# Optimization experiments

Hardware: AMD Instinct MI355X
Metric: run time of the kernel (lower is better)

Reference implementation:

```python
import jax, jax.numpy as jnp
import numpy as np

N = 20000
E = 320000
IN_FEAT = 256
HID = 256
OUT_FEAT = 128


def setup_inputs() -> dict:
    key = jax.random.key(0)
    ks = jax.random.split(key, 10)
    inp = {
        "x": jax.random.normal(ks[0], (N, IN_FEAT), dtype=jnp.float32),
        "edge_src": jax.random.randint(ks[1], (E,), 0, N, dtype=jnp.int32),
        "edge_dst": jax.random.randint(ks[2], (E,), 0, N, dtype=jnp.int32),
        "edge_w": jax.random.uniform(ks[3], (E,), dtype=jnp.float32),
        # params (Linear weights stored as [out, in], torch convention)
        "W_emb": jax.random.normal(ks[4], (HID, IN_FEAT), dtype=jnp.float32) / np.sqrt(IN_FEAT),
        "W_gc1": jax.random.normal(ks[5], (HID, 2 * HID), dtype=jnp.float32) / np.sqrt(2 * HID),
        "b_gc1": jnp.zeros((HID,), dtype=jnp.float32),
        "W_gc2": jax.random.normal(ks[6], (HID, 2 * HID), dtype=jnp.float32) / np.sqrt(2 * HID),
        "b_gc2": jnp.zeros((HID,), dtype=jnp.float32),
        "W_fc": jax.random.normal(ks[7], (OUT_FEAT, HID), dtype=jnp.float32) / np.sqrt(HID),
    }
    return inp


def reference(x, edge_src, edge_dst, edge_w, W_emb, W_gc1, b_gc1, W_gc2, b_gc2, W_fc):
    n = x.shape[0]

    def adj_mul(h):
        msgs = h[edge_src] * edge_w[:, None]           # [E, hid]
        return jax.ops.segment_sum(msgs, edge_dst, num_segments=n)

    def gconv(h, W, b):
        cat = jnp.concatenate([h, adj_mul(h)], axis=1)  # [N, 2*hid]
        return cat @ W.T + b

    h = x @ W_emb.T                                    # embedding (no bias)
    h = h + jax.nn.relu(gconv(h, W_gc1, b_gc1))        # residual (dropout = eval identity)
    h = h + jax.nn.relu(gconv(h, W_gc2, b_gc2))
    out = h @ W_fc.T                                   # fc_last (no bias)
    out = out / jnp.sqrt(jnp.sum(out * out, axis=1, keepdims=True))
    return out
```

## Files before the change

### kernel.cpp

```cpp
#include <hip/hip_runtime.h>
#include <math.h>

#define N_NODES 20000
#define E_EDGES 320000
#define HID 256
#define OUT_FEAT 128
#define MPAD 20224
#define CAP 64

#define BK 64
#define LSTR 72
#define TSTR 264

typedef __attribute__((ext_vector_type(8))) __bf16 bf16x8;
typedef __attribute__((ext_vector_type(4))) float floatx4;

__device__ __forceinline__ void write_int8_shadow(
    const __bf16 (*tile)[TSTR], int row0, int tid,
    unsigned char* __restrict__ h8, float* __restrict__ scl) {
    const int row = tid >> 3;
    const int seg = tid & 7;
    float vals[32];
    float mx = 0.f;
#pragma unroll
    for (int j = 0; j < 32; j++) {
        float v = (float)tile[row][seg * 32 + j];
        vals[j] = v;
        mx = fmaxf(mx, fabsf(v));
    }
#pragma unroll
    for (int m = 1; m <= 4; m <<= 1) mx = fmaxf(mx, __shfl_xor(mx, m));
    const float enc = mx > 0.f ? 127.f / mx : 0.f;
    unsigned int pk[8];
#pragma unroll
    for (int g = 0; g < 8; g++) {
        unsigned int wd = 0;
#pragma unroll
        for (int j = 0; j < 4; j++) {
            int q = (int)rintf(vals[g * 4 + j] * enc);
            q = q > 127 ? 127 : (q < -127 ? -127 : q);
            wd |= ((unsigned int)(q & 0xff)) << (8 * j);
        }
        pk[g] = wd;
    }
    unsigned char* dstp = h8 + (size_t)(row0 + row) * HID + seg * 32;
    *(int4*)dstp        = make_int4(pk[0], pk[1], pk[2], pk[3]);
    *(int4*)(dstp + 16) = make_int4(pk[4], pk[5], pk[6], pk[7]);
    if (seg == 0) scl[row0 + row] = mx * (1.f / 127.f);
}


#define EMB_BLK 316
#define SCAT_BLK 625
#define CONV_BLK 72

__global__ __launch_bounds__(512) void front_kernel(
    const float* __restrict__ x,
    const float* __restrict__ wembf,
    __bf16* __restrict__ hb0,
    unsigned char* __restrict__ h8,
    float* __restrict__ scl,
    const int* __restrict__ src, const int* __restrict__ dst,
    const float* __restrict__ w, int* __restrict__ counts,
    int2* __restrict__ edges,
    const float* __restrict__ w1f, const float* __restrict__ w2f,
    const float* __restrict__ wfcf,
    __bf16* __restrict__ w1b, __bf16* __restrict__ w2b,
    __bf16* __restrict__ wfcb)
{
    __shared__ __bf16 smem[64 * LSTR + 256 * LSTR];
    const int bid = blockIdx.x;
    const int tid = threadIdx.x;

    if (bid < EMB_BLK) {
        __bf16* As = smem;
        __bf16* Bs = smem + 64 * LSTR;
        const int row0 = bid * 64;
        const int wv = tid >> 6, l = tid & 63, lr = l & 15, lq = l >> 4;
        const int wm = wv & 1, wn4 = wv >> 1;

        floatx4 acc[2][4];
#pragma unroll
        for (int i = 0; i < 2; i++)
#pragma unroll
            for (int j = 0; j < 4; j++) acc[i][j] = (floatx4){0.f, 0.f, 0.f, 0.f};

        const int srow = tid >> 3;
        const int skq = (tid & 7) * 8;

        for (int kc = 0; kc < 256; kc += BK) {
            {
                int grow = row0 + srow;
                float4 v0 = make_float4(0.f, 0.f, 0.f, 0.f), v1 = v0;
                if (grow < N_NODES) {
                    const float* xp = x + (size_t)grow * HID + kc + skq;
                    v0 = *(const float4*)xp;
                    v1 = *(const float4*)(xp + 4);
                }
                bf16x8 o;
                o[0] = (__bf16)v0.x; o[1] = (__bf16)v0.y; o[2] = (__bf16)v0.z; o[3] = (__bf16)v0.w;
                o[4] = (__bf16)v1.x; o[5] = (__bf16)v1.y; o[6] = (__bf16)v1.z; o[7] = (__bf16)v1.w;
                *(bf16x8*)&As[srow * LSTR + skq] = o;
            }
#pragma unroll
            for (int r = 0; r < 4; r++) {
                int row = r * 64 + srow;
                const float* wp = wembf + (size_t)row * 256 + kc + skq;
                float4 v0 = *(const float4*)wp;
                float4 v1 = *(const float4*)(wp + 4);
                bf16x8 o;
                o[0] = (__bf16)v0.x; o[1] = (__bf16)v0.y; o[2] = (__bf16)v0.z; o[3] = (__bf16)v0.w;
                o[4] = (__bf16)v1.x; o[5] = (__bf16)v1.y; o[6] = (__bf16)v1.z; o[7] = (__bf16)v1.w;
                *(bf16x8*)&Bs[row * LSTR + skq] = o;
            }
            __syncthreads();
#pragma unroll
            for (int s = 0; s < 2; s++) {
                bf16x8 af[2], bfr[4];
#pragma unroll
                for (int mt = 0; mt < 2; mt++)
                    af[mt] = *(const bf16x8*)&As[(wm * 32 + mt * 16 + lr) * LSTR + s * 32 + lq * 8];
#pragma unroll
                for (int nt = 0; nt < 4; nt++)
                    bfr[nt] = *(const bf16x8*)&Bs[(wn4 * 64 + nt * 16 + lr) * LSTR + s * 32 + lq * 8];
#pragma unroll
                for (int mt = 0; mt < 2; mt++)
#pragma unroll
                    for (int nt = 0; nt < 4; nt++)
                        acc[mt][nt] = __builtin_amdgcn_mfma_f32_16x16x32_bf16(af[mt], bfr[nt], acc[mt][nt], 0, 0, 0);
            }
            __syncthreads();
        }
        __bf16 (*tile)[TSTR] = (__bf16(*)[TSTR])smem;
#pragma unroll
        for (int nt = 0; nt < 4; nt++) {
            const int col = wn4 * 64 + nt * 16 + lr;
#pragma unroll
            for (int mt = 0; mt < 2; mt++) {
                const int lrow = wm * 32 + mt * 16 + lq * 4;
#pragma unroll
                for (int r = 0; r < 4; r++) {
                    float v = acc[mt][nt][r];
                    hb0[(size_t)(row0 + lrow + r) * HID + col] = (__bf16)v;
                    tile[lrow + r][col] = (__bf16)v;
                }
            }
        }
        __syncthreads();
        write_int8_shadow(tile, row0, tid, h8, scl);
    } else if (bid < EMB_BLK + SCAT_BLK) {
        int e = (bid - EMB_BLK) * 512 + tid;
        int d = dst[e];
        int p = atomicAdd(&counts[d], 1);
        edges[(size_t)d * CAP + p] = make_int2(src[e], __float_as_int(w[e]));
    } else {
        const size_t gi = ((size_t)(bid - EMB_BLK - SCAT_BLK) * 512 + tid) * 8;
        const size_t s1 = 131072, s2 = 262144;
        const float* srcp; __bf16* dstp; size_t off;
        if (gi < s1)      { srcp = w1f; dstp = w1b; off = gi; }
        else if (gi < s2) { srcp = w2f; dstp = w2b; off = gi - s1; }
        else              { srcp = wfcf; dstp = wfcb; off = gi - s2; }
        float4 v0 = *(const float4*)(srcp + off);
        float4 v1 = *(const float4*)(srcp + off + 4);
        bf16x8 o;
        o[0] = (__bf16)v0.x; o[1] = (__bf16)v0.y; o[2] = (__bf16)v0.z; o[3] = (__bf16)v0.w;
        o[4] = (__bf16)v1.x; o[5] = (__bf16)v1.y; o[6] = (__bf16)v1.z; o[7] = (__bf16)v1.w;
        *(bf16x8*)(dstp + off) = o;
    }
}


__global__ __launch_bounds__(256) void aggregate_kernel(
    const unsigned char* __restrict__ h8, const float* __restrict__ scl,
    const int* __restrict__ counts,
    const int2* __restrict__ edges, __bf16* __restrict__ agg) {
    const int w = threadIdx.x >> 6, lane = threadIdx.x & 63;
    const int half = lane >> 5, lh = lane & 31;
    const int d = blockIdx.x * 8 + w * 2 + half;
    const size_t base = (size_t)d * CAP;
    const int cnt = counts[d];
    const int iters = (cnt + 15) >> 4;
    float acc[8];
#pragma unroll
    for (int q = 0; q < 8; q++) acc[q] = 0.f;

    for (int it = 0; it < iters; ++it) {
        const int jb = it * 16;
        const int2* ep = edges + base + jb;
        int4 eh[8];
#pragma unroll
        for (int u = 0; u < 8; u++) eh[u] = *(const int4*)(ep + u * 2);
        int sidx[16]; float ew[16];
#pragma unroll
        for (int u = 0; u < 8; u++) {
            const bool m0 = (jb + u * 2)     < cnt;
            const bool m1 = (jb + u * 2 + 1) < cnt;
            sidx[u * 2]     = m0 ? eh[u].x : 0;
            ew[u * 2]       = m0 ? __int_as_float(eh[u].y) : 0.f;
            sidx[u * 2 + 1] = m1 ? eh[u].z : 0;
            ew[u * 2 + 1]   = m1 ? __int_as_float(eh[u].w) : 0.f;
        }
        float ws[16];
#pragma unroll
        for (int u = 0; u < 16; u++) ws[u] = ew[u] * scl[sidx[u]];
        uint2 hv[16];
#pragma unroll
        for (int u = 0; u < 16; u++)
            hv[u] = *(const uint2*)(h8 + (size_t)sidx[u] * HID + lh * 8);
#pragma unroll
        for (int u = 0; u < 16; u++) {
            const unsigned int a = hv[u].x, b = hv[u].y;
            const float wu = ws[u];
            acc[0] = fmaf(wu, (float)(int)(signed char)(a),       acc[0]);
            acc[1] = fmaf(wu, (float)(int)(signed char)(a >> 8),  acc[1]);
            acc[2] = fmaf(wu, (float)(int)(signed char)(a >> 16), acc[2]);
            acc[3] = fmaf(wu, (float)(int)(signed char)(a >> 24), acc[3]);
            acc[4] = fmaf(wu, (float)(int)(signed char)(b),       acc[4]);
            acc[5] = fmaf(wu, (float)(int)(signed char)(b >> 8),  acc[5]);
            acc[6] = fmaf(wu, (float)(int)(signed char)(b >> 16), acc[6]);
            acc[7] = fmaf(wu, (float)(int)(signed char)(b >> 24), acc[7]);
        }
    }
    bf16x8 o;
#pragma unroll
    for (int q = 0; q < 8; q++) o[q] = (__bf16)acc[q];
    *(bf16x8*)(agg + (size_t)d * HID + lh * 8) = o;
}


__global__ __launch_bounds__(512) void gconv1_kernel(
    const __bf16* __restrict__ hp,
    const __bf16* __restrict__ ag,
    const __bf16* __restrict__ W,
    const float* __restrict__ bias,
    __bf16* __restrict__ hn,
    unsigned char* __restrict__ h8,
    float* __restrict__ scl)
{
    __shared__ __bf16 smem[64 * LSTR + 256 * LSTR];
    __bf16* As = smem;
    __bf16* Bs = smem + 64 * LSTR;
    const int tid = threadIdx.x;
    const int row0 = blockIdx.x * 64;
    const int wv = tid >> 6, l = tid & 63, lr = l & 15, lq = l >> 4;
    const int wm = wv & 1, wn4 = wv >> 1;

    floatx4 acc[2][4];
#pragma unroll
    for (int i = 0; i < 2; i++)
#pragma unroll
        for (int j = 0; j < 4; j++) acc[i][j] = (floatx4){0.f, 0.f, 0.f, 0.f};

    const int srow = tid >> 3;
    const int skq = (tid & 7) * 8;

    for (int kc = 0; kc < 512; kc += BK) {
        const __bf16* Asrc = (kc >= 256) ? ag : hp;
        const int ks = kc & 255;
        *(bf16x8*)&As[srow * LSTR + skq] =
            *(const bf16x8*)(Asrc + (size_t)(row0 + srow) * HID + ks + skq);
#pragma unroll
        for (int r = 0; r < 4; r++) {
            int row = r * 64 + srow;
            *(bf16x8*)&Bs[row * LSTR + skq] =
                *(const bf16x8*)(W + (size_t)row * 512 + kc + skq);
        }
        __syncthreads();
#pragma unroll
        for (int s = 0; s < 2; s++) {
            bf16x8 af[2], bfr[4];
#pragma unroll
            for (int mt = 0; mt < 2; mt++)
                af[mt] = *(const bf16x8*)&As[(wm * 32 + mt * 16 + lr) * LSTR + s * 32 + lq * 8];
#pragma unroll
            for (int nt = 0; nt < 4; nt++)
                bfr[nt] = *(const bf16x8*)&Bs[(wn4 * 64 + nt * 16 + lr) * LSTR + s * 32 + lq * 8];
#pragma unroll
            for (int mt = 0; mt < 2; mt++)
#pragma unroll
                for (int nt = 0; nt < 4; nt++)
                    acc[mt][nt] = __builtin_amdgcn_mfma_f32_16x16x32_bf16(af[mt], bfr[nt], acc[mt][nt], 0, 0, 0);
        }
        __syncthreads();
    }

    __bf16 (*tile)[TSTR] = (__bf16(*)[TSTR])smem;
#pragma unroll
    for (int nt = 0; nt < 4; nt++) {
        const int col = wn4 * 64 + nt * 16 + lr;
        const float b = bias[col];
#pragma unroll
        for (int mt = 0; mt < 2; mt++) {
            const int lrow = wm * 32 + mt * 16 + lq * 4;
#pragma unroll
            for (int r = 0; r < 4; r++) {
                float res = (float)hp[(size_t)(row0 + lrow + r) * HID + col];
                float v = res + fmaxf(acc[mt][nt][r] + b, 0.f);
                hn[(size_t)(row0 + lrow + r) * HID + col] = (__bf16)v;
                tile[lrow + r][col] = (__bf16)v;
            }
        }
    }
    __syncthreads();
    write_int8_shadow(tile, row0, tid, h8, scl);
}


__global__ __launch_bounds__(512) void gconv_fc_kernel(
    const __bf16* __restrict__ hp,
    const __bf16* __restrict__ ag,
    const __bf16* __restrict__ W,
    const float* __restrict__ bias,
    const __bf16* __restrict__ Wfc,
    float* __restrict__ outp)
{
    __shared__ __bf16 smem[64 * LSTR + 256 * LSTR];
    __bf16* As = smem;
    __bf16* Bs = smem + 64 * LSTR;
    const int tid = threadIdx.x;
    const int row0 = blockIdx.x * 64;
    const int wv = tid >> 6, l = tid & 63, lr = l & 15, lq = l >> 4;
    const int wm = wv & 1, wn4 = wv >> 1;

    floatx4 acc[2][4];
#pragma unroll
    for (int i = 0; i < 2; i++)
#pragma unroll
        for (int j = 0; j < 4; j++) acc[i][j] = (floatx4){0.f, 0.f, 0.f, 0.f};

    const int srow = tid >> 3;
    const int skq = (tid & 7) * 8;

    for (int kc = 0; kc < 512; kc += BK) {
        const __bf16* Asrc = (kc >= 256) ? ag : hp;
        const int ks = kc & 255;
        *(bf16x8*)&As[srow * LSTR + skq] =
            *(const bf16x8*)(Asrc + (size_t)(row0 + srow) * HID + ks + skq);
#pragma unroll
        for (int r = 0; r < 4; r++) {
            int row = r * 64 + srow;
            *(bf16x8*)&Bs[row * LSTR + skq] =
                *(const bf16x8*)(W + (size_t)row * 512 + kc + skq);
        }
        __syncthreads();
#pragma unroll
        for (int s = 0; s < 2; s++) {
            bf16x8 af[2], bfr[4];
#pragma unroll
            for (int mt = 0; mt < 2; mt++)
                af[mt] = *(const bf16x8*)&As[(wm * 32 + mt * 16 + lr) * LSTR + s * 32 + lq * 8];
#pragma unroll
            for (int nt = 0; nt < 4; nt++)
                bfr[nt] = *(const bf16x8*)&Bs[(wn4 * 64 + nt * 16 + lr) * LSTR + s * 32 + lq * 8];
#pragma unroll
            for (int mt = 0; mt < 2; mt++)
#pragma unroll
                for (int nt = 0; nt < 4; nt++)
                    acc[mt][nt] = __builtin_amdgcn_mfma_f32_16x16x32_bf16(af[mt], bfr[nt], acc[mt][nt], 0, 0, 0);
        }
        __syncthreads();
    }

    __bf16 (*tile)[TSTR] = (__bf16(*)[TSTR])smem;
#pragma unroll
    for (int nt = 0; nt < 4; nt++) {
        const int col = wn4 * 64 + nt * 16 + lr;
        const float b = bias[col];
#pragma unroll
        for (int mt = 0; mt < 2; mt++) {
            const int lrow = wm * 32 + mt * 16 + lq * 4;
#pragma unroll
            for (int r = 0; r < 4; r++) {
                float res = (float)hp[(size_t)(row0 + lrow + r) * HID + col];
                float v = res + fmaxf(acc[mt][nt][r] + b, 0.f);
                tile[lrow + r][col] = (__bf16)v;
            }
        }
    }
    __syncthreads();

    if (wv < 4) {
        floatx4 facc[8];
#pragma unroll
        for (int j = 0; j < 8; j++) facc[j] = (floatx4){0.f, 0.f, 0.f, 0.f};
#pragma unroll
        for (int kt = 0; kt < 256; kt += 32) {
            bf16x8 a = *(const bf16x8*)&tile[wv * 16 + lr][kt + lq * 8];
            bf16x8 bf8[8];
#pragma unroll
            for (int nt = 0; nt < 8; nt++)
                bf8[nt] = *(const bf16x8*)(Wfc + (size_t)(nt * 16 + lr) * 256 + kt + lq * 8);
#pragma unroll
            for (int nt = 0; nt < 8; nt++)
                facc[nt] = __builtin_amdgcn_mfma_f32_16x16x32_bf16(a, bf8[nt], facc[nt], 0, 0, 0);
        }
        float s[4];
#pragma unroll
        for (int r = 0; r < 4; r++) {
            float t = 0.f;
#pragma unroll
            for (int nt = 0; nt < 8; nt++) t = fmaf(facc[nt][r], facc[nt][r], t);
            s[r] = t;
        }
#pragma unroll
        for (int mask = 1; mask <= 8; mask <<= 1) {
#pragma unroll
            for (int r = 0; r < 4; r++) s[r] += __shfl_xor(s[r], mask);
        }
        float inv[4];
#pragma unroll
        for (int r = 0; r < 4; r++) inv[r] = rsqrtf(s[r]);
#pragma unroll
        for (int r = 0; r < 4; r++) {
            int row = row0 + wv * 16 + lq * 4 + r;
            if (row >= N_NODES) continue;
#pragma unroll
            for (int nt = 0; nt < 8; nt++)
                outp[(size_t)row * OUT_FEAT + nt * 16 + lr] = facc[nt][r] * inv[r];
        }
    }
}


extern "C" void kernel_launch(void* const* d_in, const int* in_sizes, int n_in,
                              void* d_out, int out_size, void* d_ws, size_t ws_size,
                              hipStream_t stream) {
    const float* x        = (const float*)d_in[0];
    const int*   edge_src = (const int*)d_in[1];
    const int*   edge_dst = (const int*)d_in[2];
    const float* edge_w   = (const float*)d_in[3];
    const float* W_emb    = (const float*)d_in[4];
    const float* W_gc1    = (const float*)d_in[5];
    const float* b_gc1    = (const float*)d_in[6];
    const float* W_gc2    = (const float*)d_in[7];
    const float* b_gc2    = (const float*)d_in[8];
    const float* W_fc     = (const float*)d_in[9];
    float* out = (float*)d_out;

    char* p = (char*)d_ws;
    const size_t HROW = (size_t)MPAD * HID;
    __bf16* hb0   = (__bf16*)p;             p += HROW * 2;
    __bf16* hb1   = (__bf16*)p;             p += HROW * 2;
    __bf16* aggb  = (__bf16*)p;             p += HROW * 2;
    unsigned char* h8 = (unsigned char*)p;  p += HROW;
    float*  scl   = (float*)p;              p += (size_t)MPAD * 4;
    __bf16* w1b   = (__bf16*)p;             p += 131072 * 2;
    __bf16* w2b   = (__bf16*)p;             p += 131072 * 2;
    __bf16* wfcb  = (__bf16*)p;             p += 32768 * 2;
    int2*   edges = (int2*)p;               p += (size_t)N_NODES * CAP * 8;
    int*    counts = (int*)p;               p += (size_t)MPAD * 4;

    hipMemsetAsync(counts, 0, (size_t)MPAD * 4, stream);

    front_kernel<<<EMB_BLK + SCAT_BLK + CONV_BLK, 512, 0, stream>>>(
        x, W_emb, hb0, h8, scl, edge_src, edge_dst, edge_w, counts, edges,
        W_gc1, W_gc2, W_fc, w1b, w2b, wfcb);

    aggregate_kernel<<<N_NODES / 8, 256, 0, stream>>>(h8, scl, counts, edges, aggb);

    gconv1_kernel<<<MPAD / 64, 512, 0, stream>>>(hb0, aggb, w1b, b_gc1, hb1, h8, scl);

    aggregate_kernel<<<N_NODES / 8, 256, 0, stream>>>(h8, scl, counts, edges, aggb);

    gconv_fc_kernel<<<MPAD / 64, 512, 0, stream>>>(hb1, aggb, w2b, b_gc2, wfcb, out);
}
```

Before: 202.8 us.

## Quantize aggregated features and right weight half to int8, use int8 MFMA

The aggregate kernel now writes per-row int8-quantized outputs with a float scale instead of bf16. The right (neighbour) half of each gconv weight is quantized per output row to int8 in the front kernel. The gconv GEMM splits into a bf16 MFMA pass over the self half and an int8 MFMA pass over the aggregated half, combined with the row and column scales. This halves the bytes for the aggregate buffer and the right-half weights and uses the faster int8 matrix instructions, at the cost of extra quantization error. The two gconv kernels are merged into one template.

```diff
diff --git a/kernel.cpp b/kernel.cpp
--- a/kernel.cpp
+++ b/kernel.cpp
@@ -10,10 +10,12 @@
 
 #define BK 64
 #define LSTR 72
+#define ISTR 80
 #define TSTR 264
 
 typedef __attribute__((ext_vector_type(8))) __bf16 bf16x8;
 typedef __attribute__((ext_vector_type(4))) float floatx4;
+typedef __attribute__((ext_vector_type(4))) int intx4;
 
 __device__ __forceinline__ void write_int8_shadow(
     const __bf16 (*tile)[TSTR], int row0, int tid,
@@ -52,29 +54,26 @@
 
 #define EMB_BLK 316
 #define SCAT_BLK 625
-#define CONV_BLK 72
+#define CONVL_BLK 40
+#define CONVR_BLK 64
 
 __global__ __launch_bounds__(512) void front_kernel(
-    const float* __restrict__ x,
-    const float* __restrict__ wembf,
-    __bf16* __restrict__ hb0,
-    unsigned char* __restrict__ h8,
-    float* __restrict__ scl,
+    const float* __restrict__ x, const float* __restrict__ wembf,
+    __bf16* __restrict__ hb0, unsigned char* __restrict__ h8, float* __restrict__ scl,
     const int* __restrict__ src, const int* __restrict__ dst,
-    const float* __restrict__ w, int* __restrict__ counts,
-    int2* __restrict__ edges,
-    const float* __restrict__ w1f, const float* __restrict__ w2f,
-    const float* __restrict__ wfcf,
-    __bf16* __restrict__ w1b, __bf16* __restrict__ w2b,
-    __bf16* __restrict__ wfcb)
+    const float* __restrict__ w, int* __restrict__ counts, int2* __restrict__ edges,
+    const float* __restrict__ w1f, const float* __restrict__ w2f, const float* __restrict__ wfcf,
+    __bf16* __restrict__ w1l, __bf16* __restrict__ w2l, __bf16* __restrict__ wfcb,
+    unsigned char* __restrict__ w1r8, unsigned char* __restrict__ w2r8,
+    float* __restrict__ w1rs, float* __restrict__ w2rs)
 {
-    __shared__ __bf16 smem[64 * LSTR + 256 * LSTR];
+    __shared__ char smem[64 * 144 + 256 * 144];
     const int bid = blockIdx.x;
     const int tid = threadIdx.x;
 
     if (bid < EMB_BLK) {
-        __bf16* As = smem;
-        __bf16* Bs = smem + 64 * LSTR;
+        __bf16* As = (__bf16*)smem;
+        __bf16* Bs = (__bf16*)(smem + 64 * 144);
         const int row0 = bid * 64;
         const int wv = tid >> 6, l = tid & 63, lr = l & 15, lq = l >> 4;
         const int wm = wv & 1, wn4 = wv >> 1;
@@ -153,19 +152,47 @@
         int d = dst[e];
         int p = atomicAdd(&counts[d], 1);
         edges[(size_t)d * CAP + p] = make_int2(src[e], __float_as_int(w[e]));
-    } else {
+    } else if (bid < EMB_BLK + SCAT_BLK + CONVL_BLK) {
         const size_t gi = ((size_t)(bid - EMB_BLK - SCAT_BLK) * 512 + tid) * 8;
-        const size_t s1 = 131072, s2 = 262144;
-        const float* srcp; __bf16* dstp; size_t off;
-        if (gi < s1)      { srcp = w1f; dstp = w1b; off = gi; }
-        else if (gi < s2) { srcp = w2f; dstp = w2b; off = gi - s1; }
-        else              { srcp = wfcf; dstp = wfcb; off = gi - s2; }
-        float4 v0 = *(const float4*)(srcp + off);
-        float4 v1 = *(const float4*)(srcp + off + 4);
+        const float* sp; __bf16* dp;
+        if (gi < 65536) {
+            size_t row = gi >> 8, k = gi & 255;
+            sp = w1f + row * 512 + k; dp = w1l + gi;
+        } else if (gi < 131072) {
+            size_t off = gi - 65536, row = off >> 8, k = off & 255;
+            sp = w2f + row * 512 + k; dp = w2l + off;
+        } else {
+            size_t off = gi - 131072;
+            sp = wfcf + off; dp = wfcb + off;
+        }
+        float4 v0 = *(const float4*)sp;
+        float4 v1 = *(const float4*)(sp + 4);
         bf16x8 o;
         o[0] = (__bf16)v0.x; o[1] = (__bf16)v0.y; o[2] = (__bf16)v0.z; o[3] = (__bf16)v0.w;
         o[4] = (__bf16)v1.x; o[5] = (__bf16)v1.y; o[6] = (__bf16)v1.z; o[7] = (__bf16)v1.w;
-        *(bf16x8*)(dstp + off) = o;
+        *(bf16x8*)dp = o;
+    } else {
+        const int gw = (bid - EMB_BLK - SCAT_BLK - CONVL_BLK) * 8 + (tid >> 6);
+        const int lane = tid & 63;
+        const float* Wsrc = (gw < 256) ? w1f : w2f;
+        unsigned char* d8 = (gw < 256) ? w1r8 : w2r8;
+        float* ds = (gw < 256) ? w1rs : w2rs;
+        const int r = gw & 255;
+        float4 v = *(const float4*)(Wsrc + (size_t)r * 512 + 256 + lane * 4);
+        float mx = fmaxf(fmaxf(fabsf(v.x), fabsf(v.y)), fmaxf(fabsf(v.z), fabsf(v.w)));
+#pragma unroll
+        for (int m = 1; m <= 32; m <<= 1) mx = fmaxf(mx, __shfl_xor(mx, m));
+        const float enc = mx > 0.f ? 127.f / mx : 0.f;
+        unsigned int wd = 0;
+        float vv[4] = {v.x, v.y, v.z, v.w};
+#pragma unroll
+        for (int j = 0; j < 4; j++) {
+            int q = (int)rintf(vv[j] * enc);
+            q = q > 127 ? 127 : (q < -127 ? -127 : q);
+            wd |= ((unsigned int)(q & 0xff)) << (8 * j);
+        }
+        *(unsigned int*)(d8 + (size_t)r * 256 + lane * 4) = wd;
+        if (lane == 0) ds[r] = mx * (1.f / 127.f);
     }
 }
 
@@ -173,7 +200,8 @@
 __global__ __launch_bounds__(256) void aggregate_kernel(
     const unsigned char* __restrict__ h8, const float* __restrict__ scl,
     const int* __restrict__ counts,
-    const int2* __restrict__ edges, __bf16* __restrict__ agg) {
+    const int2* __restrict__ edges,
+    unsigned char* __restrict__ agg8, float* __restrict__ ascl) {
     const int w = threadIdx.x >> 6, lane = threadIdx.x & 63;
     const int half = lane >> 5, lh = lane & 31;
     const int d = blockIdx.x * 8 + w * 2 + half;
@@ -221,49 +249,68 @@
             acc[7] = fmaf(wu, (float)(int)(signed char)(b >> 24), acc[7]);
         }
     }
-    bf16x8 o;
-#pragma unroll
-    for (int q = 0; q < 8; q++) o[q] = (__bf16)acc[q];
-    *(bf16x8*)(agg + (size_t)d * HID + lh * 8) = o;
+    float mx = 0.f;
+#pragma unroll
+    for (int q = 0; q < 8; q++) mx = fmaxf(mx, fabsf(acc[q]));
+#pragma unroll
+    for (int m = 1; m <= 16; m <<= 1) mx = fmaxf(mx, __shfl_xor(mx, m));
+    const float enc = mx > 0.f ? 127.f / mx : 0.f;
+    unsigned int w0 = 0, w1v = 0;
+#pragma unroll
+    for (int j = 0; j < 4; j++) {
+        int q0 = (int)rintf(acc[j] * enc);
+        q0 = q0 > 127 ? 127 : (q0 < -127 ? -127 : q0);
+        w0 |= ((unsigned int)(q0 & 0xff)) << (8 * j);
+        int q1 = (int)rintf(acc[4 + j] * enc);
+        q1 = q1 > 127 ? 127 : (q1 < -127 ? -127 : q1);
+        w1v |= ((unsigned int)(q1 & 0xff)) << (8 * j);
+    }
+    *(uint2*)(agg8 + (size_t)d * HID + lh * 8) = make_uint2(w0, w1v);
+    if (lh == 0) ascl[d] = mx * (1.f / 127.f);
 }
 
 
-__global__ __launch_bounds__(512) void gconv1_kernel(
+template <bool LAST>
+__global__ __launch_bounds__(512) void gconv_kernel(
     const __bf16* __restrict__ hp,
-    const __bf16* __restrict__ ag,
-    const __bf16* __restrict__ W,
+    const unsigned char* __restrict__ ag8, const float* __restrict__ ascl,
+    const __bf16* __restrict__ Wl,
+    const unsigned char* __restrict__ Wr8, const float* __restrict__ Wrs,
     const float* __restrict__ bias,
-    __bf16* __restrict__ hn,
-    unsigned char* __restrict__ h8,
-    float* __restrict__ scl)
+    __bf16* __restrict__ hn, unsigned char* __restrict__ h8, float* __restrict__ scl,
+    const __bf16* __restrict__ Wfc, float* __restrict__ outp)
 {
-    __shared__ __bf16 smem[64 * LSTR + 256 * LSTR];
-    __bf16* As = smem;
-    __bf16* Bs = smem + 64 * LSTR;
+    __shared__ char smem[64 * 144 + 256 * 144];
+    __bf16* As = (__bf16*)smem;
+    __bf16* Bs = (__bf16*)(smem + 64 * 144);
+    char* As8 = smem;
+    char* Bs8 = smem + 64 * ISTR;
     const int tid = threadIdx.x;
     const int row0 = blockIdx.x * 64;
     const int wv = tid >> 6, l = tid & 63, lr = l & 15, lq = l >> 4;
     const int wm = wv & 1, wn4 = wv >> 1;
 
     floatx4 acc[2][4];
+    intx4 acc8[2][4];
 #pragma unroll
     for (int i = 0; i < 2; i++)
 #pragma unroll
-        for (int j = 0; j < 4; j++) acc[i][j] = (floatx4){0.f, 0.f, 0.f, 0.f};
+        for (int j = 0; j < 4; j++) {
+            acc[i][j] = (floatx4){0.f, 0.f, 0.f, 0.f};
+            acc8[i][j] = (intx4){0, 0, 0, 0};
+        }
 
     const int srow = tid >> 3;
     const int skq = (tid & 7) * 8;
 
-    for (int kc = 0; kc < 512; kc += BK) {
-        const __bf16* Asrc = (kc >= 256) ? ag : hp;
-        const int ks = kc & 255;
+    for (int kc = 0; kc < 256; kc += BK) {
         *(bf16x8*)&As[srow * LSTR + skq] =
-            *(const bf16x8*)(Asrc + (size_t)(row0 + srow) * HID + ks + skq);
+            *(const bf16x8*)(hp + (size_t)(row0 + srow) * HID + kc + skq);
 #pragma unroll
         for (int r = 0; r < 4; r++) {
             int row = r * 64 + srow;
             *(bf16x8*)&Bs[row * LSTR + skq] =
-                *(const bf16x8*)(W + (size_t)row * 512 + kc + skq);
+                *(const bf16x8*)(Wl + (size_t)row * 256 + kc + skq);
         }
         __syncthreads();
 #pragma unroll
@@ -281,6 +328,35 @@
                 for (int nt = 0; nt < 4; nt++)
                     acc[mt][nt] = __builtin_amdgcn_mfma_f32_16x16x32_bf16(af[mt], bfr[nt], acc[mt][nt], 0, 0, 0);
         }
+        __syncthreads();
+    }
+
+    for (int kc = 0; kc < 256; kc += BK) {
+        {
+            int row = tid >> 3, sg = (tid & 7) * 8;
+            *(uint2*)&As8[row * ISTR + sg] =
+                *(const uint2*)(ag8 + (size_t)(row0 + row) * HID + kc + sg);
+        }
+#pragma unroll
+        for (int rr = 0; rr < 2; rr++) {
+            int idx = rr * 512 + tid;
+            int row = idx >> 2, sg = (idx & 3) * 16;
+            *(int4*)&Bs8[row * ISTR + sg] =
+                *(const int4*)(Wr8 + (size_t)row * 256 + kc + sg);
+        }
+        __syncthreads();
+        intx4 a8[2], b8[4];
+#pragma unroll
+        for (int mt = 0; mt < 2; mt++)
+            a8[mt] = *(const intx4*)&As8[(wm * 32 + mt * 16 + lr) * ISTR + lq * 16];
+#pragma unroll
+        for (int nt = 0; nt < 4; nt++)
+            b8[nt] = *(const intx4*)&Bs8[(wn4 * 64 + nt * 16 + lr) * ISTR + lq * 16];
+#pragma unroll
+        for (int mt = 0; mt < 2; mt++)
+#pragma unroll
+            for (int nt = 0; nt < 4; nt++)
+                acc8[mt][nt] = __builtin_amdgcn_mfma_i32_16x16x64_i8(a8[mt], b8[nt], acc8[mt][nt], 0, 0, 0);
         __syncthreads();
     }
 
@@ -289,97 +365,26 @@
     for (int nt = 0; nt < 4; nt++) {
         const int col = wn4 * 64 + nt * 16 + lr;
         const float b = bias[col];
+        const float wrc = Wrs[col];
 #pragma unroll
         for (int mt = 0; mt < 2; mt++) {
             const int lrow = wm * 32 + mt * 16 + lq * 4;
 #pragma unroll
             for (int r = 0; r < 4; r++) {
-                float res = (float)hp[(size_t)(row0 + lrow + r) * HID + col];
-                float v = res + fmaxf(acc[mt][nt][r] + b, 0.f);
-                hn[(size_t)(row0 + lrow + r) * HID + col] = (__bf16)v;
+                const int row = row0 + lrow + r;
+                float gem = acc[mt][nt][r] + (float)acc8[mt][nt][r] * (ascl[row] * wrc);
+                float res = (float)hp[(size_t)row * HID + col];
+                float v = res + fmaxf(gem + b, 0.f);
+                if (!LAST) hn[(size_t)row * HID + col] = (__bf16)v;
                 tile[lrow + r][col] = (__bf16)v;
             }
         }
     }
     __syncthreads();
-    write_int8_shadow(tile, row0, tid, h8, scl);
-}
-
-
-__global__ __launch_bounds__(512) void gconv_fc_kernel(
-    const __bf16* __restrict__ hp,
-    const __bf16* __restrict__ ag,
-    const __bf16* __restrict__ W,
-    const float* __restrict__ bias,
-    const __bf16* __restrict__ Wfc,
-    float* __restrict__ outp)
-{
-    __shared__ __bf16 smem[64 * LSTR + 256 * LSTR];
-    __bf16* As = smem;
-    __bf16* Bs = smem + 64 * LSTR;
-    const int tid = threadIdx.x;
-    const int row0 = blockIdx.x * 64;
-    const int wv = tid >> 6, l = tid & 63, lr = l & 15, lq = l >> 4;
-    const int wm = wv & 1, wn4 = wv >> 1;
-
-    floatx4 acc[2][4];
-#pragma unroll
-    for (int i = 0; i < 2; i++)
-#pragma unroll
-        for (int j = 0; j < 4; j++) acc[i][j] = (floatx4){0.f, 0.f, 0.f, 0.f};
-
-    const int srow = tid >> 3;
-    const int skq = (tid & 7) * 8;
-
-    for (int kc = 0; kc < 512; kc += BK) {
-        const __bf16* Asrc = (kc >= 256) ? ag : hp;
-        const int ks = kc & 255;
-        *(bf16x8*)&As[srow * LSTR + skq] =
-            *(const bf16x8*)(Asrc + (size_t)(row0 + srow) * HID + ks + skq);
-#pragma unroll
-        for (int r = 0; r < 4; r++) {
-            int row = r * 64 + srow;
-            *(bf16x8*)&Bs[row * LSTR + skq] =
-                *(const bf16x8*)(W + (size_t)row * 512 + kc + skq);
-        }
-        __syncthreads();
-#pragma unroll
-        for (int s = 0; s < 2; s++) {
-            bf16x8 af[2], bfr[4];
-#pragma unroll
-            for (int mt = 0; mt < 2; mt++)
-                af[mt] = *(const bf16x8*)&As[(wm * 32 + mt * 16 + lr) * LSTR + s * 32 + lq * 8];
-#pragma unroll
-            for (int nt = 0; nt < 4; nt++)
-                bfr[nt] = *(const bf16x8*)&Bs[(wn4 * 64 + nt * 16 + lr) * LSTR + s * 32 + lq * 8];
-#pragma unroll
-            for (int mt = 0; mt < 2; mt++)
-#pragma unroll
-                for (int nt = 0; nt < 4; nt++)
-                    acc[mt][nt] = __builtin_amdgcn_mfma_f32_16x16x32_bf16(af[mt], bfr[nt], acc[mt][nt], 0, 0, 0);
-        }
-        __syncthreads();
-    }
-
-    __bf16 (*tile)[TSTR] = (__bf16(*)[TSTR])smem;
-#pragma unroll
-    for (int nt = 0; nt < 4; nt++) {
-        const int col = wn4 * 64 + nt * 16 + lr;
-        const float b = bias[col];
-#pragma unroll
-        for (int mt = 0; mt < 2; mt++) {
-            const int lrow = wm * 32 + mt * 16 + lq * 4;
-#pragma unroll
-            for (int r = 0; r < 4; r++) {
-                float res = (float)hp[(size_t)(row0 + lrow + r) * HID + col];
-                float v = res + fmaxf(acc[mt][nt][r] + b, 0.f);
-                tile[lrow + r][col] = (__bf16)v;
-            }
-        }
-    }
-    __syncthreads();
-
-    if (wv < 4) {
+
+    if (!LAST) {
+        write_int8_shadow(tile, row0, tid, h8, scl);
+    } else if (wv < 4) {
         floatx4 facc[8];
 #pragma unroll
         for (int j = 0; j < 8; j++) facc[j] = (floatx4){0.f, 0.f, 0.f, 0.f};
@@ -441,26 +446,33 @@
     const size_t HROW = (size_t)MPAD * HID;
     __bf16* hb0   = (__bf16*)p;             p += HROW * 2;
     __bf16* hb1   = (__bf16*)p;             p += HROW * 2;
-    __bf16* aggb  = (__bf16*)p;             p += HROW * 2;
     unsigned char* h8 = (unsigned char*)p;  p += HROW;
     float*  scl   = (float*)p;              p += (size_t)MPAD * 4;
-    __bf16* w1b   = (__bf16*)p;             p += 131072 * 2;
-    __bf16* w2b   = (__bf16*)p;             p += 131072 * 2;
+    unsigned char* agg8 = (unsigned char*)p; p += HROW;
+    float*  ascl  = (float*)p;              p += (size_t)MPAD * 4;
+    __bf16* w1l   = (__bf16*)p;             p += 65536 * 2;
+    __bf16* w2l   = (__bf16*)p;             p += 65536 * 2;
     __bf16* wfcb  = (__bf16*)p;             p += 32768 * 2;
+    unsigned char* w1r8 = (unsigned char*)p; p += 65536;
+    unsigned char* w2r8 = (unsigned char*)p; p += 65536;
+    float*  w1rs  = (float*)p;              p += 256 * 4;
+    float*  w2rs  = (float*)p;              p += 256 * 4;
     int2*   edges = (int2*)p;               p += (size_t)N_NODES * CAP * 8;
     int*    counts = (int*)p;               p += (size_t)MPAD * 4;
 
     hipMemsetAsync(counts, 0, (size_t)MPAD * 4, stream);
 
-    front_kernel<<<EMB_BLK + SCAT_BLK + CONV_BLK, 512, 0, stream>>>(
+    front_kernel<<<EMB_BLK + SCAT_BLK + CONVL_BLK + CONVR_BLK, 512, 0, stream>>>(
         x, W_emb, hb0, h8, scl, edge_src, edge_dst, edge_w, counts, edges,
-        W_gc1, W_gc2, W_fc, w1b, w2b, wfcb);
-
-    aggregate_kernel<<<N_NODES / 8, 256, 0, stream>>>(h8, scl, counts, edges, aggb);
-
-    gconv1_kernel<<<MPAD / 64, 512, 0, stream>>>(hb0, aggb, w1b, b_gc1, hb1, h8, scl);
-
-    aggregate_kernel<<<N_NODES / 8, 256, 0, stream>>>(h8, scl, counts, edges, aggb);
-
-    gconv_fc_kernel<<<MPAD / 64, 512, 0, stream>>>(hb1, aggb, w2b, b_gc2, wfcb, out);
+        W_gc1, W_gc2, W_fc, w1l, w2l, wfcb, w1r8, w2r8, w1rs, w2rs);
+
+    aggregate_kernel<<<N_NODES / 8, 256, 0, stream>>>(h8, scl, counts, edges, agg8, ascl);
+
+    gconv_kernel<false><<<MPAD / 64, 512, 0, stream>>>(
+        hb0, agg8, ascl, w1l, w1r8, w1rs, b_gc1, hb1, h8, scl, nullptr, nullptr);
+
+    aggregate_kernel<<<N_NODES / 8, 256, 0, stream>>>(h8, scl, counts, edges, agg8, ascl);
+
+    gconv_kernel<true><<<MPAD / 64, 512, 0, stream>>>(
+        hb1, agg8, ascl, w2l, w2r8, w2rs, b_gc2, nullptr, nullptr, nullptr, wfcb, out);
 }
```

New measurement: 202.5 us. Within noise of the previous version (-0.1%).

## Overlap edge aggregation with identity-half GEMM in a combined kernel

Applied to the files above, without the earlier changes.

Each graph-conv layer's GEMM is split into two halves. The half that multiplies h by the left 256 columns of W has no dependence on the aggregation, so it now runs as extra blocks inside the aggregation kernel and writes fp32 partial sums to a new workspace buffer. The follow-up kernel computes only the aggregated half and adds the partials before bias, ReLU and residual, which lets the GEMM overlap with the memory-latency-bound gather. The cost is an extra fp32 round-trip of an N×256 buffer, and the aggregation waves now process 8 edges per iteration instead of 16.

```diff
diff --git a/kernel.cpp b/kernel.cpp
--- a/kernel.cpp
+++ b/kernel.cpp
@@ -55,18 +55,12 @@
 #define CONV_BLK 72
 
 __global__ __launch_bounds__(512) void front_kernel(
-    const float* __restrict__ x,
-    const float* __restrict__ wembf,
-    __bf16* __restrict__ hb0,
-    unsigned char* __restrict__ h8,
-    float* __restrict__ scl,
+    const float* __restrict__ x, const float* __restrict__ wembf,
+    __bf16* __restrict__ hb0, unsigned char* __restrict__ h8, float* __restrict__ scl,
     const int* __restrict__ src, const int* __restrict__ dst,
-    const float* __restrict__ w, int* __restrict__ counts,
-    int2* __restrict__ edges,
-    const float* __restrict__ w1f, const float* __restrict__ w2f,
-    const float* __restrict__ wfcf,
-    __bf16* __restrict__ w1b, __bf16* __restrict__ w2b,
-    __bf16* __restrict__ wfcb)
+    const float* __restrict__ w, int* __restrict__ counts, int2* __restrict__ edges,
+    const float* __restrict__ w1f, const float* __restrict__ w2f, const float* __restrict__ wfcf,
+    __bf16* __restrict__ w1b, __bf16* __restrict__ w2b, __bf16* __restrict__ wfcb)
 {
     __shared__ __bf16 smem[64 * LSTR + 256 * LSTR];
     const int bid = blockIdx.x;
@@ -156,86 +150,152 @@
     } else {
         const size_t gi = ((size_t)(bid - EMB_BLK - SCAT_BLK) * 512 + tid) * 8;
         const size_t s1 = 131072, s2 = 262144;
-        const float* srcp; __bf16* dstp; size_t off;
-        if (gi < s1)      { srcp = w1f; dstp = w1b; off = gi; }
-        else if (gi < s2) { srcp = w2f; dstp = w2b; off = gi - s1; }
-        else              { srcp = wfcf; dstp = wfcb; off = gi - s2; }
-        float4 v0 = *(const float4*)(srcp + off);
-        float4 v1 = *(const float4*)(srcp + off + 4);
+        const float* sp; __bf16* dp; size_t off;
+        if (gi < s1)      { sp = w1f; dp = w1b; off = gi; }
+        else if (gi < s2) { sp = w2f; dp = w2b; off = gi - s1; }
+        else              { sp = wfcf; dp = wfcb; off = gi - s2; }
+        float4 v0 = *(const float4*)(sp + off);
+        float4 v1 = *(const float4*)(sp + off + 4);
         bf16x8 o;
         o[0] = (__bf16)v0.x; o[1] = (__bf16)v0.y; o[2] = (__bf16)v0.z; o[3] = (__bf16)v0.w;
         o[4] = (__bf16)v1.x; o[5] = (__bf16)v1.y; o[6] = (__bf16)v1.z; o[7] = (__bf16)v1.w;
-        *(bf16x8*)(dstp + off) = o;
+        *(bf16x8*)(dp + off) = o;
     }
 }
 
 
-__global__ __launch_bounds__(256) void aggregate_kernel(
+#define AGG_BLK 1250
+
+__global__ __launch_bounds__(512) void agg_gemmL_kernel(
     const unsigned char* __restrict__ h8, const float* __restrict__ scl,
-    const int* __restrict__ counts,
-    const int2* __restrict__ edges, __bf16* __restrict__ agg) {
-    const int w = threadIdx.x >> 6, lane = threadIdx.x & 63;
-    const int half = lane >> 5, lh = lane & 31;
-    const int d = blockIdx.x * 8 + w * 2 + half;
-    const size_t base = (size_t)d * CAP;
-    const int cnt = counts[d];
-    const int iters = (cnt + 15) >> 4;
-    float acc[8];
-#pragma unroll
-    for (int q = 0; q < 8; q++) acc[q] = 0.f;
-
-    for (int it = 0; it < iters; ++it) {
-        const int jb = it * 16;
-        const int2* ep = edges + base + jb;
-        int4 eh[8];
-#pragma unroll
-        for (int u = 0; u < 8; u++) eh[u] = *(const int4*)(ep + u * 2);
-        int sidx[16]; float ew[16];
-#pragma unroll
-        for (int u = 0; u < 8; u++) {
-            const bool m0 = (jb + u * 2)     < cnt;
-            const bool m1 = (jb + u * 2 + 1) < cnt;
-            sidx[u * 2]     = m0 ? eh[u].x : 0;
-            ew[u * 2]       = m0 ? __int_as_float(eh[u].y) : 0.f;
-            sidx[u * 2 + 1] = m1 ? eh[u].z : 0;
-            ew[u * 2 + 1]   = m1 ? __int_as_float(eh[u].w) : 0.f;
-        }
-        float ws[16];
-#pragma unroll
-        for (int u = 0; u < 16; u++) ws[u] = ew[u] * scl[sidx[u]];
-        uint2 hv[16];
-#pragma unroll
-        for (int u = 0; u < 16; u++)
-            hv[u] = *(const uint2*)(h8 + (size_t)sidx[u] * HID + lh * 8);
-#pragma unroll
-        for (int u = 0; u < 16; u++) {
-            const unsigned int a = hv[u].x, b = hv[u].y;
-            const float wu = ws[u];
-            acc[0] = fmaf(wu, (float)(int)(signed char)(a),       acc[0]);
-            acc[1] = fmaf(wu, (float)(int)(signed char)(a >> 8),  acc[1]);
-            acc[2] = fmaf(wu, (float)(int)(signed char)(a >> 16), acc[2]);
-            acc[3] = fmaf(wu, (float)(int)(signed char)(a >> 24), acc[3]);
-            acc[4] = fmaf(wu, (float)(int)(signed char)(b),       acc[4]);
-            acc[5] = fmaf(wu, (float)(int)(signed char)(b >> 8),  acc[5]);
-            acc[6] = fmaf(wu, (float)(int)(signed char)(b >> 16), acc[6]);
-            acc[7] = fmaf(wu, (float)(int)(signed char)(b >> 24), acc[7]);
-        }
-    }
-    bf16x8 o;
-#pragma unroll
-    for (int q = 0; q < 8; q++) o[q] = (__bf16)acc[q];
-    *(bf16x8*)(agg + (size_t)d * HID + lh * 8) = o;
+    const int* __restrict__ counts, const int2* __restrict__ edges,
+    __bf16* __restrict__ aggb,
+    const __bf16* __restrict__ hp,
+    const __bf16* __restrict__ W,
+    float* __restrict__ pacc)
+{
+    __shared__ __bf16 smem[64 * LSTR + 256 * LSTR];
+    const int tid = threadIdx.x;
+
+    if (blockIdx.x < AGG_BLK) {
+        const int wave = tid >> 6, lane = tid & 63;
+        const int half = lane >> 5, lh = lane & 31;
+        const int d = blockIdx.x * 16 + wave * 2 + half;
+        const size_t base = (size_t)d * CAP;
+        const int cnt = counts[d];
+        const int iters = (cnt + 7) >> 3;
+        float acc[8];
+#pragma unroll
+        for (int q = 0; q < 8; q++) acc[q] = 0.f;
+
+        for (int it = 0; it < iters; ++it) {
+            const int jb = it * 8;
+            const int2* ep = edges + base + jb;
+            int4 eh[4];
+#pragma unroll
+            for (int u = 0; u < 4; u++) eh[u] = *(const int4*)(ep + u * 2);
+            int sidx[8]; float ew[8];
+#pragma unroll
+            for (int u = 0; u < 4; u++) {
+                const bool m0 = (jb + u * 2)     < cnt;
+                const bool m1 = (jb + u * 2 + 1) < cnt;
+                sidx[u * 2]     = m0 ? eh[u].x : 0;
+                ew[u * 2]       = m0 ? __int_as_float(eh[u].y) : 0.f;
+                sidx[u * 2 + 1] = m1 ? eh[u].z : 0;
+                ew[u * 2 + 1]   = m1 ? __int_as_float(eh[u].w) : 0.f;
+            }
+            float ws8[8];
+#pragma unroll
+            for (int u = 0; u < 8; u++) ws8[u] = ew[u] * scl[sidx[u]];
+            uint2 hv[8];
+#pragma unroll
+            for (int u = 0; u < 8; u++)
+                hv[u] = *(const uint2*)(h8 + (size_t)sidx[u] * HID + lh * 8);
+#pragma unroll
+            for (int u = 0; u < 8; u++) {
+                const unsigned int a = hv[u].x, b = hv[u].y;
+                const float wu = ws8[u];
+                acc[0] = fmaf(wu, (float)(int)(signed char)(a),       acc[0]);
+                acc[1] = fmaf(wu, (float)(int)(signed char)(a >> 8),  acc[1]);
+                acc[2] = fmaf(wu, (float)(int)(signed char)(a >> 16), acc[2]);
+                acc[3] = fmaf(wu, (float)(int)(signed char)(a >> 24), acc[3]);
+                acc[4] = fmaf(wu, (float)(int)(signed char)(b),       acc[4]);
+                acc[5] = fmaf(wu, (float)(int)(signed char)(b >> 8),  acc[5]);
+                acc[6] = fmaf(wu, (float)(int)(signed char)(b >> 16), acc[6]);
+                acc[7] = fmaf(wu, (float)(int)(signed char)(b >> 24), acc[7]);
+            }
+        }
+        bf16x8 o;
+#pragma unroll
+        for (int q = 0; q < 8; q++) o[q] = (__bf16)acc[q];
+        *(bf16x8*)(aggb + (size_t)d * HID + lh * 8) = o;
+    } else {
+        __bf16* As = smem;
+        __bf16* Bs = smem + 64 * LSTR;
+        const int row0 = (blockIdx.x - AGG_BLK) * 64;
+        const int wv = tid >> 6, l = tid & 63, lr = l & 15, lq = l >> 4;
+        const int wm = wv & 1, wn4 = wv >> 1;
+
+        floatx4 acc[2][4];
+#pragma unroll
+        for (int i = 0; i < 2; i++)
+#pragma unroll
+            for (int j = 0; j < 4; j++) acc[i][j] = (floatx4){0.f, 0.f, 0.f, 0.f};
+
+        const int srow = tid >> 3;
+        const int skq = (tid & 7) * 8;
+
+        for (int kc = 0; kc < 256; kc += BK) {
+            *(bf16x8*)&As[srow * LSTR + skq] =
+                *(const bf16x8*)(hp + (size_t)(row0 + srow) * HID + kc + skq);
+#pragma unroll
+            for (int r = 0; r < 4; r++) {
+                int row = r * 64 + srow;
+                *(bf16x8*)&Bs[row * LSTR + skq] =
+                    *(const bf16x8*)(W + (size_t)row * 512 + kc + skq);
+            }
+            __syncthreads();
+#pragma unroll
+            for (int s = 0; s < 2; s++) {
+                bf16x8 af[2], bfr[4];
+#pragma unroll
+                for (int mt = 0; mt < 2; mt++)
+                    af[mt] = *(const bf16x8*)&As[(wm * 32 + mt * 16 + lr) * LSTR + s * 32 + lq * 8];
+#pragma unroll
+                for (int nt = 0; nt < 4; nt++)
+                    bfr[nt] = *(const bf16x8*)&Bs[(wn4 * 64 + nt * 16 + lr) * LSTR + s * 32 + lq * 8];
+#pragma unroll
+                for (int mt = 0; mt < 2; mt++)
+#pragma unroll
+                    for (int nt = 0; nt < 4; nt++)
+                        acc[mt][nt] = __builtin_amdgcn_mfma_f32_16x16x32_bf16(af[mt], bfr[nt], acc[mt][nt], 0, 0, 0);
+            }
+            __syncthreads();
+        }
+#pragma unroll
+        for (int nt = 0; nt < 4; nt++) {
+            const int col = wn4 * 64 + nt * 16 + lr;
+#pragma unroll
+            for (int mt = 0; mt < 2; mt++) {
+                const int lrow = wm * 32 + mt * 16 + lq * 4;
+#pragma unroll
+                for (int r = 0; r < 4; r++)
+                    pacc[(size_t)(row0 + lrow + r) * HID + col] = acc[mt][nt][r];
+            }
+        }
+    }
 }
 
 
-__global__ __launch_bounds__(512) void gconv1_kernel(
+template <bool LAST>
+__global__ __launch_bounds__(512) void gconvR_kernel(
     const __bf16* __restrict__ hp,
     const __bf16* __restrict__ ag,
     const __bf16* __restrict__ W,
+    const float* __restrict__ pacc,
     const float* __restrict__ bias,
-    __bf16* __restrict__ hn,
-    unsigned char* __restrict__ h8,
-    float* __restrict__ scl)
+    __bf16* __restrict__ hn, unsigned char* __restrict__ h8, float* __restrict__ scl,
+    const __bf16* __restrict__ Wfc, float* __restrict__ outp)
 {
     __shared__ __bf16 smem[64 * LSTR + 256 * LSTR];
     __bf16* As = smem;
@@ -254,16 +314,14 @@
     const int srow = tid >> 3;
     const int skq = (tid & 7) * 8;
 
-    for (int kc = 0; kc < 512; kc += BK) {
-        const __bf16* Asrc = (kc >= 256) ? ag : hp;
-        const int ks = kc & 255;
+    for (int kc = 0; kc < 256; kc += BK) {
         *(bf16x8*)&As[srow * LSTR + skq] =
-            *(const bf16x8*)(Asrc + (size_t)(row0 + srow) * HID + ks + skq);
+            *(const bf16x8*)(ag + (size_t)(row0 + srow) * HID + kc + skq);
 #pragma unroll
         for (int r = 0; r < 4; r++) {
             int row = r * 64 + srow;
             *(bf16x8*)&Bs[row * LSTR + skq] =
-                *(const bf16x8*)(W + (size_t)row * 512 + kc + skq);
+                *(const bf16x8*)(W + (size_t)row * 512 + 256 + kc + skq);
         }
         __syncthreads();
 #pragma unroll
@@ -294,92 +352,20 @@
             const int lrow = wm * 32 + mt * 16 + lq * 4;
 #pragma unroll
             for (int r = 0; r < 4; r++) {
-                float res = (float)hp[(size_t)(row0 + lrow + r) * HID + col];
-                float v = res + fmaxf(acc[mt][nt][r] + b, 0.f);
-                hn[(size_t)(row0 + lrow + r) * HID + col] = (__bf16)v;
+                const int row = row0 + lrow + r;
+                float gem = acc[mt][nt][r] + pacc[(size_t)row * HID + col];
+                float res = (float)hp[(size_t)row * HID + col];
+                float v = res + fmaxf(gem + b, 0.f);
+                if (!LAST) hn[(size_t)row * HID + col] = (__bf16)v;
                 tile[lrow + r][col] = (__bf16)v;
             }
         }
     }
     __syncthreads();
-    write_int8_shadow(tile, row0, tid, h8, scl);
-}
-
-
-__global__ __launch_bounds__(512) void gconv_fc_kernel(
-    const __bf16* __restrict__ hp,
-    const __bf16* __restrict__ ag,
-    const __bf16* __restrict__ W,
-    const float* __restrict__ bias,
-    const __bf16* __restrict__ Wfc,
-    float* __restrict__ outp)
-{
-    __shared__ __bf16 smem[64 * LSTR + 256 * LSTR];
-    __bf16* As = smem;
-    __bf16* Bs = smem + 64 * LSTR;
-    const int tid = threadIdx.x;
-    const int row0 = blockIdx.x * 64;
-    const int wv = tid >> 6, l = tid & 63, lr = l & 15, lq = l >> 4;
-    const int wm = wv & 1, wn4 = wv >> 1;
-
-    floatx4 acc[2][4];
-#pragma unroll
-    for (int i = 0; i < 2; i++)
-#pragma unroll
-        for (int j = 0; j < 4; j++) acc[i][j] = (floatx4){0.f, 0.f, 0.f, 0.f};
-
-    const int srow = tid >> 3;
-    const int skq = (tid & 7) * 8;
-
-    for (int kc = 0; kc < 512; kc += BK) {
-        const __bf16* Asrc = (kc >= 256) ? ag : hp;
-        const int ks = kc & 255;
-        *(bf16x8*)&As[srow * LSTR + skq] =
-            *(const bf16x8*)(Asrc + (size_t)(row0 + srow) * HID + ks + skq);
-#pragma unroll
-        for (int r = 0; r < 4; r++) {
-            int row = r * 64 + srow;
-            *(bf16x8*)&Bs[row * LSTR + skq] =
-                *(const bf16x8*)(W + (size_t)row * 512 + kc + skq);
-        }
-        __syncthreads();
-#pragma unroll
-        for (int s = 0; s < 2; s++) {
-            bf16x8 af[2], bfr[4];
-#pragma unroll
-            for (int mt = 0; mt < 2; mt++)
-                af[mt] = *(const bf16x8*)&As[(wm * 32 + mt * 16 + lr) * LSTR + s * 32 + lq * 8];
-#pragma unroll
-            for (int nt = 0; nt < 4; nt++)
-                bfr[nt] = *(const bf16x8*)&Bs[(wn4 * 64 + nt * 16 + lr) * LSTR + s * 32 + lq * 8];
-#pragma unroll
-            for (int mt = 0; mt < 2; mt++)
-#pragma unroll
-                for (int nt = 0; nt < 4; nt++)
-                    acc[mt][nt] = __builtin_amdgcn_mfma_f32_16x16x32_bf16(af[mt], bfr[nt], acc[mt][nt], 0, 0, 0);
-        }
-        __syncthreads();
-    }
-
-    __bf16 (*tile)[TSTR] = (__bf16(*)[TSTR])smem;
-#pragma unroll
-    for (int nt = 0; nt < 4; nt++) {
-        const int col = wn4 * 64 + nt * 16 + lr;
-        const float b = bias[col];
-#pragma unroll
-        for (int mt = 0; mt < 2; mt++) {
-            const int lrow = wm * 32 + mt * 16 + lq * 4;
-#pragma unroll
-            for (int r = 0; r < 4; r++) {
-                float res = (float)hp[(size_t)(row0 + lrow + r) * HID + col];
-                float v = res + fmaxf(acc[mt][nt][r] + b, 0.f);
-                tile[lrow + r][col] = (__bf16)v;
-            }
-        }
-    }
-    __syncthreads();
-
-    if (wv < 4) {
+
+    if (!LAST) {
+        write_int8_shadow(tile, row0, tid, h8, scl);
+    } else if (wv < 4) {
         floatx4 facc[8];
 #pragma unroll
         for (int j = 0; j < 8; j++) facc[j] = (floatx4){0.f, 0.f, 0.f, 0.f};
@@ -444,6 +430,7 @@
     __bf16* aggb  = (__bf16*)p;             p += HROW * 2;
     unsigned char* h8 = (unsigned char*)p;  p += HROW;
     float*  scl   = (float*)p;              p += (size_t)MPAD * 4;
+    float*  pacc  = (float*)p;              p += HROW * 4;
     __bf16* w1b   = (__bf16*)p;             p += 131072 * 2;
     __bf16* w2b   = (__bf16*)p;             p += 131072 * 2;
     __bf16* wfcb  = (__bf16*)p;             p += 32768 * 2;
@@ -456,11 +443,15 @@
         x, W_emb, hb0, h8, scl, edge_src, edge_dst, edge_w, counts, edges,
         W_gc1, W_gc2, W_fc, w1b, w2b, wfcb);
 
-    aggregate_kernel<<<N_NODES / 8, 256, 0, stream>>>(h8, scl, counts, edges, aggb);
-
-    gconv1_kernel<<<MPAD / 64, 512, 0, stream>>>(hb0, aggb, w1b, b_gc1, hb1, h8, scl);
-
-    aggregate_kernel<<<N_NODES / 8, 256, 0, stream>>>(h8, scl, counts, edges, aggb);
-
-    gconv_fc_kernel<<<MPAD / 64, 512, 0, stream>>>(hb1, aggb, w2b, b_gc2, wfcb, out);
+    agg_gemmL_kernel<<<AGG_BLK + 316, 512, 0, stream>>>(
+        h8, scl, counts, edges, aggb, hb0, w1b, pacc);
+
+    gconvR_kernel<false><<<316, 512, 0, stream>>>(
+        hb0, aggb, w1b, pacc, b_gc1, hb1, h8, scl, nullptr, nullptr);
+
+    agg_gemmL_kernel<<<AGG_BLK + 316, 512, 0, stream>>>(
+        h8, scl, counts, edges, aggb, hb1, w2b, pacc);
+
+    gconvR_kernel<true><<<316, 512, 0, stream>>>(
+        hb1, aggb, w2b, pacc, b_gc2, nullptr, nullptr, nullptr, wfcb, out);
 }
```

Measured after the change: 207.4 us. +2.3%, slower.
